# Optimization experiments

Measured on AMD Instinct MI355X. Metric: run time of the kernel, lower is better.

The kernel has to match this reference:

```python
import jax, jax.numpy as jnp
import numpy as np

B, S, D = 4, 2048, 512
H, HD, RL = 8, 64, 64   # nheads, head_dim = D//H, rl_dim
TEMPER = 1.0
BETA = 1.0
SLOPE = 0.01  # LeakyReLU negative slope
LN_EPS = 1e-5


def setup_inputs() -> dict:
    key = jax.random.key(0)
    ks = jax.random.split(key, 12)
    scale = 0.02
    return {
        "h":   jax.random.normal(ks[0], (B, S, D), dtype=jnp.float32),
        "rh":  jax.random.normal(ks[1], (B, S, RL), dtype=jnp.float32),
        "Wl":  jax.random.normal(ks[2], (D, D), dtype=jnp.float32) * scale,   # linear_l (in,out)
        "Wr":  jax.random.normal(ks[3], (D, D), dtype=jnp.float32) * scale,   # linear_r
        "al":  jax.random.normal(ks[4], (HD,), dtype=jnp.float32) * scale,    # att_l: Linear(head_dim,1)
        "ar":  jax.random.normal(ks[5], (HD,), dtype=jnp.float32) * scale,    # att_r
        "Wrs": jax.random.normal(ks[6], (RL, RL * H), dtype=jnp.float32) * scale,  # r_source
        "Wrt": jax.random.normal(ks[7], (RL, RL * H), dtype=jnp.float32) * scale,  # r_target
        "Wf":  jax.random.normal(ks[8], (D, D), dtype=jnp.float32) * scale,   # linear_final
        "ln_g": jnp.ones((D,), dtype=jnp.float32),
        "ln_b": jnp.zeros((D,), dtype=jnp.float32),
    }


def _layer_norm(x, g, b):
    mu = jnp.mean(x, axis=-1, keepdims=True)
    var = jnp.mean(jnp.square(x - mu), axis=-1, keepdims=True)
    return (x - mu) * jax.lax.rsqrt(var + LN_EPS) * g + b


def reference(h, rh, Wl, Wr, al, ar, Wrs, Wrt, Wf, ln_g, ln_b):
    leaky = lambda x: jnp.where(x >= 0, x, SLOPE * x)
    # projections -> [B, H, S, HD]
    fl = (h @ Wl).reshape(B, S, H, HD).transpose(0, 2, 1, 3)
    fr = (h @ Wr).reshape(B, S, H, HD).transpose(0, 2, 1, 3)
    # additive attention logits: [B,H,S,1] + [B,H,1,S]
    sl = jnp.einsum('bhsd,d->bhs', leaky(fl), al)
    sr = jnp.einsum('bhsd,d->bhs', leaky(fr), ar)
    score = sl[:, :, :, None] + sr[:, :, None, :]
    # relation-embedding bilinear bias: r_k @ r_q -> [B,H,S,S]
    r_k = (rh @ Wrs).reshape(B, S, H, RL).transpose(0, 2, 1, 3)   # [B,H,S,RL]
    r_q = (rh @ Wrt).reshape(B, S, H, RL).transpose(0, 2, 3, 1)   # [B,H,RL,S]
    score = score + BETA * jnp.einsum('bhsr,bhrt->bhst', r_k, r_q)
    score = jax.nn.softmax(score / TEMPER, axis=-1)
    # context and output projection (dropout = 0 -> identity)
    context = jnp.einsum('bhst,bhtd->bhsd', score, fr)
    h_sa = context.transpose(0, 2, 1, 3).reshape(B, S, H * HD)
    fh = h_sa @ Wf
    return _layer_norm(h + fh, ln_g, ln_b)
```

## Files before the change

### kernel.cpp

```cpp
#include <hip/hip_runtime.h>
#include <math.h>

#define B_ 4
#define S_ 2048
#define D_ 512
#define H_ 8
#define HD_ 64
#define RL_ 64
#define LN_EPS 1e-5f
#define SLOPE 0.01f
#define LOG2E 1.4426950408889634f

typedef __attribute__((ext_vector_type(8))) __bf16 bf16x8;
typedef __attribute__((ext_vector_type(4))) float f32x4;

__device__ __forceinline__ float leaky(float x) { return x >= 0.f ? x : SLOPE * x; }

__device__ __forceinline__ ushort f2bf(float f) {
    union { float f; unsigned u; } v; v.f = f;
    unsigned r = v.u + 0x7fffu + ((v.u >> 16) & 1u);
    return (ushort)(r >> 16);
}
__device__ __forceinline__ unsigned fbits(float f) {
    union { float f; unsigned u; } v; v.f = f; return v.u;
}

__device__ __forceinline__ void g2lds16(const void* g, void* l) {
    __builtin_amdgcn_global_load_lds(
        (const __attribute__((address_space(1))) void*)(uintptr_t)g,
        (__attribute__((address_space(3))) void*)(uintptr_t)l, 16, 0, 0);
}

__global__ __launch_bounds__(256) void prep(
    const float* __restrict__ h, const float* __restrict__ rh,
    const float* __restrict__ Wr, const float* __restrict__ Wf,
    const float* __restrict__ Wrs, const float* __restrict__ Wrt,
    ushort* __restrict__ hb, ushort* __restrict__ rhb,
    ushort* __restrict__ WrT, ushort* __restrict__ WfT,
    ushort* __restrict__ WrsT, ushort* __restrict__ WrtT)
{
    const int bx = blockIdx.x, tid = threadIdx.x;
    if (bx < 4608) {
        const float* in = (bx < 4096) ? h : rh;
        ushort* o = (bx < 4096) ? hb : rhb;
        const int i = (bx < 4096 ? bx : bx - 4096) * 256 + tid;
        const float4 v = ((const float4*)in)[i];
        ushort4 u; u.x = f2bf(v.x); u.y = f2bf(v.y); u.z = f2bf(v.z); u.w = f2bf(v.w);
        ((ushort4*)o)[i] = u;
        return;
    }
    __shared__ float TS[64][65];
    int t = bx - 4608;
    const float* in; ushort* out; int K, tk, tn;
    if (t < 64)       { in = Wr;  out = WrT;  K = 512; tk = t & 7; tn = t >> 3; }
    else if (t < 128) { in = Wf;  out = WfT;  K = 512; t -= 64; tk = t & 7; tn = t >> 3; }
    else if (t < 136) { in = Wrs; out = WrsT; K = 64;  tk = 0; tn = t - 128; }
    else              { in = Wrt; out = WrtT; K = 64;  tk = 0; tn = t - 136; }
    const int k0 = tk * 64, n0 = tn * 64;
    const int r = tid >> 4, c4 = (tid & 15) * 4;
    #pragma unroll
    for (int p = 0; p < 4; ++p) {
        const int row = r + 16 * p;
        const float4 v = *(const float4*)(in + (size_t)(k0 + row) * 512 + n0 + c4);
        TS[row][c4] = v.x; TS[row][c4 + 1] = v.y;
        TS[row][c4 + 2] = v.z; TS[row][c4 + 3] = v.w;
    }
    __syncthreads();
    #pragma unroll
    for (int p = 0; p < 4; ++p) {
        const int nn = r + 16 * p;
        ushort4 o;
        o.x = f2bf(TS[c4 + 0][nn]); o.y = f2bf(TS[c4 + 1][nn]);
        o.z = f2bf(TS[c4 + 2][nn]); o.w = f2bf(TS[c4 + 3][nn]);
        *(ushort4*)(out + (size_t)(n0 + nn) * K + k0 + c4) = o;
    }
}

__global__ __launch_bounds__(256) void proj(
    const ushort* __restrict__ hb, const ushort* __restrict__ rhb,
    const ushort* __restrict__ WrT, const ushort* __restrict__ WrsT,
    const ushort* __restrict__ WrtT,
    ushort* __restrict__ frT, ushort* __restrict__ rkw, ushort* __restrict__ rqw,
    float* __restrict__ sred, const float* __restrict__ ar)
{
    __shared__ ushort As[2][64 * 32];
    __shared__ ushort Bs[2][128 * 32];

    const int tid = threadIdx.x;
    const int lane = tid & 63, w = tid >> 6;
    const int ln = lane & 15, quad = lane >> 4;
    const int wm = w >> 1, wn = w & 1;
    const int m0 = blockIdx.x * 64, n0 = blockIdx.y * 128;
    const int z = blockIdx.z;

    const ushort* A; const ushort* wt; ushort* co; float scl; int K;
    if (z == 0)      { A = hb;  wt = WrT;  co = frT; scl = LOG2E; K = 512; }
    else if (z == 1) { A = rhb; wt = WrsT; co = rkw; scl = LOG2E; K = 64; }
    else             { A = rhb; wt = WrtT; co = rqw; scl = 1.0f;  K = 64; }

    const int srA = tid >> 2;
    const int lchA = ((lane & 3) - (srA >> 1)) & 3;
    const ushort* AgB = A + (size_t)(m0 + srA) * K + lchA * 8;
    const int srB = w * 32 + (lane >> 2);
    const int lchB = ((lane & 3) - (srB >> 1)) & 3;
    const ushort* BgB0 = wt + (size_t)(n0 + srB) * K + lchB * 8;
    const ushort* BgB1 = BgB0 + (size_t)16 * K;
    const int aoff = tid * 8;
    const int boff = srB * 32 + (lane & 3) * 8;
    const int pc = (quad + (ln >> 1)) & 3;

    g2lds16(AgB, &As[0][aoff]);
    g2lds16(BgB0, &Bs[0][boff]);
    g2lds16(BgB1, &Bs[0][boff + 512]);

    f32x4 acc[2][4] = {};
    int buf = 0;
    for (int k0 = 0; k0 < K; k0 += 32) {
        __syncthreads();
        if (k0 + 32 < K) {
            g2lds16(AgB + k0 + 32, &As[buf ^ 1][aoff]);
            g2lds16(BgB0 + k0 + 32, &Bs[buf ^ 1][boff]);
            g2lds16(BgB1 + k0 + 32, &Bs[buf ^ 1][boff + 512]);
        }
        bf16x8 af[2], bfr[4];
        #pragma unroll
        for (int mi = 0; mi < 2; ++mi)
            af[mi] = *(const bf16x8*)&As[buf][(wm * 32 + mi * 16 + ln) * 32 + pc * 8];
        #pragma unroll
        for (int ni = 0; ni < 4; ++ni)
            bfr[ni] = *(const bf16x8*)&Bs[buf][(wn * 64 + ni * 16 + ln) * 32 + pc * 8];
        #pragma unroll
        for (int mi = 0; mi < 2; ++mi)
            #pragma unroll
            for (int ni = 0; ni < 4; ++ni)
                acc[mi][ni] = __builtin_amdgcn_mfma_f32_16x16x32_bf16(
                    af[mi], bfr[ni], acc[mi][ni], 0, 0, 0);
        buf ^= 1;
    }

    const int head = blockIdx.y * 2 + wn;
    const int b = m0 >> 11;
    const size_t bh = (size_t)b * H_ + head;
    if (z == 0) {
        #pragma unroll
        for (int mi = 0; mi < 2; ++mi) {
            const int s = (m0 & (S_ - 1)) + wm * 32 + mi * 16 + quad * 4;
            #pragma unroll
            for (int ni = 0; ni < 4; ++ni) {
                const int d = ni * 16 + ln;
                ushort4 o;
                o.x = f2bf(acc[mi][ni][0]); o.y = f2bf(acc[mi][ni][1]);
                o.z = f2bf(acc[mi][ni][2]); o.w = f2bf(acc[mi][ni][3]);
                *(ushort4*)(co + (bh * 64 + d) * S_ + s) = o;
            }
        }
        float a4[4];
        #pragma unroll
        for (int ni = 0; ni < 4; ++ni) a4[ni] = ar[ni * 16 + ln];
        #pragma unroll
        for (int mi = 0; mi < 2; ++mi) {
            const int s = (m0 & (S_ - 1)) + wm * 32 + mi * 16 + quad * 4;
            #pragma unroll
            for (int r = 0; r < 4; ++r) {
                float v = 0.f;
                #pragma unroll
                for (int ni = 0; ni < 4; ++ni)
                    v += leaky(acc[mi][ni][r]) * a4[ni];
                #pragma unroll
                for (int off = 8; off; off >>= 1) v += __shfl_xor(v, off, 16);
                if (ln == 0) sred[bh * S_ + s + r] = v * scl;
            }
        }
    } else {
        #pragma unroll
        for (int mi = 0; mi < 2; ++mi) {
            const int s = (m0 & (S_ - 1)) + wm * 32 + mi * 16 + quad * 4;
            #pragma unroll
            for (int ni = 0; ni < 4; ++ni) {
                const int d = ni * 16 + ln;
                #pragma unroll
                for (int r = 0; r < 4; ++r)
                    co[(bh * S_ + s + r) * 64 + d] = f2bf(acc[mi][ni][r] * scl);
            }
        }
    }
}

#define WAITV(N) asm volatile("s_waitcnt vmcnt(" #N ")" ::: "memory")
#define BARR()   __builtin_amdgcn_s_barrier()

__global__ __launch_bounds__(128, 2) void attn_mfma(
    const ushort* __restrict__ frT, const ushort* __restrict__ rk,
    const ushort* __restrict__ rq, const float* __restrict__ sr,
    ushort* __restrict__ hsa)
{
    __shared__ ushort RQ[2][64][64];
    __shared__ ushort FT[2][64][64];
    __shared__ ushort PS[4][16][64];

    const int tid = threadIdx.x;
    const int w = tid >> 6;
    const int lane = tid & 63;
    const int ln = lane & 15;
    const int quad = lane >> 4;

    const int flat = blockIdx.x + 32 * (blockIdx.y + 8 * blockIdx.z);
    const int wid = (flat & 7) * 128 + (flat >> 3);
    const int q0 = (wid & 31) * 64;
    const int h = (wid >> 5) & 7;
    const int b = wid >> 8;
    const size_t bh = (size_t)b * H_ + h;

    bf16x8 a[2][2];
    #pragma unroll
    for (int qs = 0; qs < 2; ++qs) {
        const ushort* p = rk + ((bh * S_ + q0 + 32 * w + 16 * qs + ln) << 6);
        a[qs][0] = *(const bf16x8*)(p + quad * 8);
        a[qs][1] = *(const bf16x8*)(p + 32 + quad * 8);
    }

    const ushort* rq_g = rq + (bh * S_ << 6);
    const ushort* ft_g = frT + (size_t)bh * 64 * S_;
    const float* srp = sr + bh * S_;

    const int rl = lane >> 3;
    const int pg = lane & 7;
    const int base_row = w * 32 + rl;
    const int sgF = (pg - rl) & 7;

    #define STAGE(BUF, t0)                                                    \
        {                                                                     \
            _Pragma("unroll")                                                 \
            for (int m = 0; m < 4; ++m) {                                     \
                const int rr = base_row + 8 * m;                              \
                const int sgR = (pg - ((rr >> 2) & 7)) & 7;                   \
                g2lds16(rq_g + ((size_t)((t0) + rr) << 6) + sgR * 8,          \
                        &RQ[BUF][rr][pg * 8]);                                \
                g2lds16(ft_g + (size_t)rr * S_ + (t0) + sgF * 8,              \
                        &FT[BUF][rr][pg * 8]);                                \
            }                                                                 \
        }

    const ushort* rqrA = &RQ[0][0][0] + 4 * ln * 64 + ((quad + ln) & 7) * 8;
    const ushort* rqrB = &RQ[0][0][0] + 4 * ln * 64 + ((quad + 4 + ln) & 7) * 8;
    const ushort* ftrA = &FT[0][0][0] + ln * 64 + ((quad + ln) & 7) * 8;
    const ushort* ftrB = &FT[0][0][0] + ln * 64 + ((quad + 4 + ln) & 7) * 8;
    ushort* sb[2];
    sb[0] = &PS[w * 2][0][0]; sb[1] = &PS[w * 2 + 1][0][0];
    int wr_off[4];
    #pragma unroll
    for (int r = 0; r < 4; ++r) {
        const int prow = quad * 4 + r;
        wr_off[r] = prow * 64 + (((ln >> 1) + prow) & 7) * 8 + (ln & 1) * 4;
    }
    const int rd0 = ln * 64 + ((quad + ln) & 7) * 8;
    const int rd1 = ln * 64 + ((quad + 4 + ln) & 7) * 8;

    float lsum[2][4] = {};
    f32x4 ctx[2][4] = {};

    #define COMPUTE(BI, SV)                                                        \
        {                                                                          \
            f32x4 sc[2][4];                                                        \
            _Pragma("unroll")                                                      \
            for (int jb = 0; jb < 4; ++jb) {                                       \
                const bf16x8 b0 = *(const bf16x8*)(rqrA + (BI) * 4096 + jb * 64);  \
                const bf16x8 b1 = *(const bf16x8*)(rqrB + (BI) * 4096 + jb * 64);  \
                _Pragma("unroll")                                                  \
                for (int qs = 0; qs < 2; ++qs) {                                   \
                    f32x4 tt = {0.f, 0.f, 0.f, 0.f};                               \
                    tt = __builtin_amdgcn_mfma_f32_16x16x32_bf16(a[qs][0], b0, tt, 0, 0, 0); \
                    tt = __builtin_amdgcn_mfma_f32_16x16x32_bf16(a[qs][1], b1, tt, 0, 0, 0); \
                    sc[qs][jb] = tt;                                               \
                }                                                                  \
            }                                                                      \
            _Pragma("unroll")                                                      \
            for (int qs = 0; qs < 2; ++qs)                                         \
                _Pragma("unroll")                                                  \
                for (int r = 0; r < 4; ++r) {                                      \
                    const float p0 = __builtin_amdgcn_exp2f(sc[qs][0][r] + SV.x);  \
                    const float p1 = __builtin_amdgcn_exp2f(sc[qs][1][r] + SV.y);  \
                    const float p2 = __builtin_amdgcn_exp2f(sc[qs][2][r] + SV.z);  \
                    const float p3 = __builtin_amdgcn_exp2f(sc[qs][3][r] + SV.w);  \
                    lsum[qs][r] += (p0 + p1) + (p2 + p3);                          \
                    const unsigned lo = (fbits(p0) >> 16) | (fbits(p1) & 0xffff0000u); \
                    const unsigned hi = (fbits(p2) >> 16) | (fbits(p3) & 0xffff0000u); \
                    *(uint2*)(sb[qs] + wr_off[r]) = make_uint2(lo, hi);            \
                }                                                                  \
            const bf16x8 pa00 = *(const bf16x8*)(sb[0] + rd0);                     \
            const bf16x8 pa01 = *(const bf16x8*)(sb[0] + rd1);                     \
            const bf16x8 pa10 = *(const bf16x8*)(sb[1] + rd0);                     \
            const bf16x8 pa11 = *(const bf16x8*)(sb[1] + rd1);                     \
            _Pragma("unroll")                                                      \
            for (int jb = 0; jb < 4; ++jb) {                                       \
                const bf16x8 fb0 = *(const bf16x8*)(ftrA + (BI) * 4096 + jb * 1024); \
                const bf16x8 fb1 = *(const bf16x8*)(ftrB + (BI) * 4096 + jb * 1024); \
                ctx[0][jb] = __builtin_amdgcn_mfma_f32_16x16x32_bf16(pa00, fb0, ctx[0][jb], 0, 0, 0); \
                ctx[0][jb] = __builtin_amdgcn_mfma_f32_16x16x32_bf16(pa01, fb1, ctx[0][jb], 0, 0, 0); \
                ctx[1][jb] = __builtin_amdgcn_mfma_f32_16x16x32_bf16(pa10, fb0, ctx[1][jb], 0, 0, 0); \
                ctx[1][jb] = __builtin_amdgcn_mfma_f32_16x16x32_bf16(pa11, fb1, ctx[1][jb], 0, 0, 0); \
            }                                                                      \
        }

    float4 sv0, sv1;
    STAGE(0, 0)  sv0 = *(const float4*)(srp + 0 + 4 * ln);

    for (int it = 0; it < 15; ++it) {
        const int t0 = it * 128;
        WAITV(0); BARR();
        STAGE(1, t0 + 64)   sv1 = *(const float4*)(srp + t0 + 64 + 4 * ln);
        COMPUTE(0, sv0)
        WAITV(0); BARR();
        STAGE(0, t0 + 128)  sv0 = *(const float4*)(srp + t0 + 128 + 4 * ln);
        COMPUTE(1, sv1)
    }
    WAITV(0); BARR();
    STAGE(1, 1984)  sv1 = *(const float4*)(srp + 1984 + 4 * ln);
    COMPUTE(0, sv0)
    WAITV(0); BARR();
    COMPUTE(1, sv1)

    #pragma unroll
    for (int qs = 0; qs < 2; ++qs)
        #pragma unroll
        for (int r = 0; r < 4; ++r) {
            float l = lsum[qs][r];
            #pragma unroll
            for (int off = 8; off; off >>= 1) l += __shfl_xor(l, off, 16);
            const float inv = 1.f / l;
            const int q = q0 + 32 * w + 16 * qs + quad * 4 + r;
            ushort* orow = hsa + (size_t)(b * S_ + q) * D_ + h * 64;
            #pragma unroll
            for (int jb = 0; jb < 4; ++jb)
                orow[16 * jb + ln] = f2bf(ctx[qs][jb][r] * inv);
        }
}

__global__ __launch_bounds__(256) void gemm_out(
    const ushort* __restrict__ A, const ushort* __restrict__ WT,
    float* __restrict__ C)
{
    __shared__ ushort As[2][64 * 32];
    __shared__ ushort Bs[2][128 * 32];

    const int tid = threadIdx.x;
    const int lane = tid & 63, w = tid >> 6;
    const int ln = lane & 15, quad = lane >> 4;
    const int wm = w >> 1, wn = w & 1;
    const int m0 = blockIdx.x * 64, n0 = blockIdx.y * 128;
    const int K = 512;

    const int srA = tid >> 2;
    const int lchA = ((lane & 3) - (srA >> 1)) & 3;
    const ushort* AgB = A + (size_t)(m0 + srA) * K + lchA * 8;
    const int srB = w * 32 + (lane >> 2);
    const int lchB = ((lane & 3) - (srB >> 1)) & 3;
    const ushort* BgB0 = WT + (size_t)(n0 + srB) * K + lchB * 8;
    const ushort* BgB1 = BgB0 + (size_t)16 * K;
    const int aoff = tid * 8;
    const int boff = srB * 32 + (lane & 3) * 8;
    const int pc = (quad + (ln >> 1)) & 3;

    g2lds16(AgB, &As[0][aoff]);
    g2lds16(BgB0, &Bs[0][boff]);
    g2lds16(BgB1, &Bs[0][boff + 512]);

    f32x4 acc[2][4] = {};
    int buf = 0;
    for (int k0 = 0; k0 < K; k0 += 32) {
        __syncthreads();
        if (k0 + 32 < K) {
            g2lds16(AgB + k0 + 32, &As[buf ^ 1][aoff]);
            g2lds16(BgB0 + k0 + 32, &Bs[buf ^ 1][boff]);
            g2lds16(BgB1 + k0 + 32, &Bs[buf ^ 1][boff + 512]);
        }
        bf16x8 af[2], bfr[4];
        #pragma unroll
        for (int mi = 0; mi < 2; ++mi)
            af[mi] = *(const bf16x8*)&As[buf][(wm * 32 + mi * 16 + ln) * 32 + pc * 8];
        #pragma unroll
        for (int ni = 0; ni < 4; ++ni)
            bfr[ni] = *(const bf16x8*)&Bs[buf][(wn * 64 + ni * 16 + ln) * 32 + pc * 8];
        #pragma unroll
        for (int mi = 0; mi < 2; ++mi)
            #pragma unroll
            for (int ni = 0; ni < 4; ++ni)
                acc[mi][ni] = __builtin_amdgcn_mfma_f32_16x16x32_bf16(
                    af[mi], bfr[ni], acc[mi][ni], 0, 0, 0);
        buf ^= 1;
    }

    #pragma unroll
    for (int mi = 0; mi < 2; ++mi) {
        const int row = m0 + wm * 32 + mi * 16 + quad * 4;
        #pragma unroll
        for (int ni = 0; ni < 4; ++ni) {
            const int col = n0 + wn * 64 + ni * 16 + ln;
            #pragma unroll
            for (int r = 0; r < 4; ++r)
                C[(size_t)(row + r) * 512 + col] = acc[mi][ni][r];
        }
    }
}

__global__ __launch_bounds__(256) void ln_kernel(
    const float* __restrict__ h, const float* __restrict__ fh,
    const float* __restrict__ g, const float* __restrict__ bb,
    float* __restrict__ out)
{
    const int row = blockIdx.x, tid = threadIdx.x;
    const float* hp = h + (size_t)row * 512;
    const float* fp = fh + (size_t)row * 512;
    const float x0 = hp[tid] + fp[tid];
    const float x1 = hp[tid + 256] + fp[tid + 256];
    __shared__ float red[4];

    float s = x0 + x1;
    #pragma unroll
    for (int off = 32; off; off >>= 1) s += __shfl_xor(s, off, 64);
    if ((tid & 63) == 0) red[tid >> 6] = s;
    __syncthreads();
    const float mu = (red[0] + red[1] + red[2] + red[3]) * (1.f / 512.f);

    const float d0 = x0 - mu, d1 = x1 - mu;
    float v = d0 * d0 + d1 * d1;
    #pragma unroll
    for (int off = 32; off; off >>= 1) v += __shfl_xor(v, off, 64);
    __syncthreads();
    if ((tid & 63) == 0) red[tid >> 6] = v;
    __syncthreads();
    const float var = (red[0] + red[1] + red[2] + red[3]) * (1.f / 512.f);
    const float inv = rsqrtf(var + LN_EPS);

    out[(size_t)row * 512 + tid] = d0 * inv * g[tid] + bb[tid];
    out[(size_t)row * 512 + tid + 256] = d1 * inv * g[tid + 256] + bb[tid + 256];
}

extern "C" void kernel_launch(void* const* d_in, const int* in_sizes, int n_in,
                              void* d_out, int out_size, void* d_ws, size_t ws_size,
                              hipStream_t stream)
{
    const float* h   = (const float*)d_in[0];
    const float* rh  = (const float*)d_in[1];
    const float* Wr  = (const float*)d_in[3];
    const float* ar  = (const float*)d_in[5];
    const float* Wrs = (const float*)d_in[6];
    const float* Wrt = (const float*)d_in[7];
    const float* Wf  = (const float*)d_in[8];
    const float* lng = (const float*)d_in[9];
    const float* lnb = (const float*)d_in[10];
    float* out = (float*)d_out;
    char* wsb  = (char*)d_ws;

    const size_t MB = (size_t)1 << 20;
    ushort* hb   = (ushort*)(wsb);
    ushort* rhb  = (ushort*)(wsb + 8 * MB);
    ushort* WrT  = (ushort*)(wsb + 9 * MB);
    ushort* WfT  = (ushort*)(wsb + 9 * MB + 512 * 1024);
    ushort* WrsT = (ushort*)(wsb + 10 * MB);
    ushort* WrtT = (ushort*)(wsb + 10 * MB + 64 * 1024);
    ushort* frT  = (ushort*)(wsb + 11 * MB);
    ushort* rkw  = (ushort*)(wsb + 19 * MB);
    ushort* rqw  = (ushort*)(wsb + 27 * MB);
    float*  sr   = (float*) (wsb + 35 * MB);
    ushort* hsab = (ushort*)(wsb + 36 * MB);
    float*  fh   = (float*) (wsb + 44 * MB);

    dim3 blk(256);
    prep<<<dim3(4752), blk, 0, stream>>>(h, rh, Wr, Wf, Wrs, Wrt,
                                         hb, rhb, WrT, WfT, WrsT, WrtT);
    proj<<<dim3(128, 4, 3), blk, 0, stream>>>(hb, rhb, WrT, WrsT, WrtT,
                                              frT, rkw, rqw, sr, ar);
    attn_mfma<<<dim3(S_ / 64, H_, B_), dim3(128), 0, stream>>>(frT, rkw, rqw, sr, hsab);
    gemm_out<<<dim3(128, 4), blk, 0, stream>>>(hsab, WfT, fh);
    ln_kernel<<<dim3(B_ * S_), blk, 0, stream>>>(h, fh, lng, lnb, out);
}
```

Measured before the change: 176.7 us.

## Rewrite attention core with 32x32x16 MFMA and register-resident probabilities

The attention kernel moves from 16x16x32 to 32x32x16 bf16 MFMA tiles. Each wave now handles 64 queries, and each block handles 128 queries, so the grid is halved. Score tiles are computed transposed so the exponentiated probabilities can be packed to bf16 and fed straight into the P@V MFMA through a permlane32 swap, instead of a round trip through LDS. The projection kernel permutes its frT store order to match the new operand layout. This adds register pressure and drops the launch-bounds occupancy hint from 2 to 1, with fewer blocks available to hide latency.

Result: slower. 197.2 us (+11.6%).

```diff
diff --git a/kernel.cpp b/kernel.cpp
--- a/kernel.cpp
+++ b/kernel.cpp
@@ -13,6 +13,7 @@
 
 typedef __attribute__((ext_vector_type(8))) __bf16 bf16x8;
 typedef __attribute__((ext_vector_type(4))) float f32x4;
+typedef __attribute__((ext_vector_type(16))) float f32x16;
 
 __device__ __forceinline__ float leaky(float x) { return x >= 0.f ? x : SLOPE * x; }
 
@@ -21,14 +22,18 @@
     unsigned r = v.u + 0x7fffu + ((v.u >> 16) & 1u);
     return (ushort)(r >> 16);
 }
-__device__ __forceinline__ unsigned fbits(float f) {
-    union { float f; unsigned u; } v; v.f = f; return v.u;
+__device__ __forceinline__ unsigned pk2bf(float a, float b) {
+    return (unsigned)f2bf(a) | ((unsigned)f2bf(b) << 16);
 }
 
 __device__ __forceinline__ void g2lds16(const void* g, void* l) {
     __builtin_amdgcn_global_load_lds(
         (const __attribute__((address_space(1))) void*)(uintptr_t)g,
         (__attribute__((address_space(3))) void*)(uintptr_t)l, 16, 0, 0);
+}
+
+__device__ __forceinline__ void plane32swap(unsigned &x, unsigned &y) {
+    asm volatile("v_permlane32_swap_b32 %0, %1" : "+v"(x), "+v"(y));
 }
 
 __global__ __launch_bounds__(256) void prep(
@@ -145,13 +150,14 @@
         #pragma unroll
         for (int mi = 0; mi < 2; ++mi) {
             const int s = (m0 & (S_ - 1)) + wm * 32 + mi * 16 + quad * 4;
+            const int sp = (s & ~15) | ((((0x1320u >> (quad * 4)) & 0xFu)) << 2);
             #pragma unroll
             for (int ni = 0; ni < 4; ++ni) {
                 const int d = ni * 16 + ln;
                 ushort4 o;
                 o.x = f2bf(acc[mi][ni][0]); o.y = f2bf(acc[mi][ni][1]);
                 o.z = f2bf(acc[mi][ni][2]); o.w = f2bf(acc[mi][ni][3]);
-                *(ushort4*)(co + (bh * 64 + d) * S_ + s) = o;
+                *(ushort4*)(co + (bh * 64 + d) * S_ + sp) = o;
             }
         }
         float a4[4];
@@ -189,151 +195,147 @@
 #define WAITV(N) asm volatile("s_waitcnt vmcnt(" #N ")" ::: "memory")
 #define BARR()   __builtin_amdgcn_s_barrier()
 
-__global__ __launch_bounds__(128, 2) void attn_mfma(
+__global__ __launch_bounds__(128, 1) void attn_mfma(
     const ushort* __restrict__ frT, const ushort* __restrict__ rk,
     const ushort* __restrict__ rq, const float* __restrict__ sr,
     ushort* __restrict__ hsa)
 {
     __shared__ ushort RQ[2][64][64];
     __shared__ ushort FT[2][64][64];
-    __shared__ ushort PS[4][16][64];
 
     const int tid = threadIdx.x;
     const int w = tid >> 6;
     const int lane = tid & 63;
-    const int ln = lane & 15;
-    const int quad = lane >> 4;
-
-    const int flat = blockIdx.x + 32 * (blockIdx.y + 8 * blockIdx.z);
-    const int wid = (flat & 7) * 128 + (flat >> 3);
-    const int q0 = (wid & 31) * 64;
-    const int h = (wid >> 5) & 7;
-    const int b = wid >> 8;
+    const int lq = lane & 31;
+    const int hi = lane >> 5;
+
+    const int flat = blockIdx.x + 16 * (blockIdx.y + 8 * blockIdx.z);
+    const int wid = (flat & 7) * 64 + (flat >> 3);
+    const int q0 = (wid & 15) * 128;
+    const int h = (wid >> 4) & 7;
+    const int b = wid >> 7;
     const size_t bh = (size_t)b * H_ + h;
-
-    bf16x8 a[2][2];
-    #pragma unroll
-    for (int qs = 0; qs < 2; ++qs) {
-        const ushort* p = rk + ((bh * S_ + q0 + 32 * w + 16 * qs + ln) << 6);
-        a[qs][0] = *(const bf16x8*)(p + quad * 8);
-        a[qs][1] = *(const bf16x8*)(p + 32 + quad * 8);
+    const int qb = q0 + 64 * w;
+
+    bf16x8 bq[2][4];
+    #pragma unroll
+    for (int qt = 0; qt < 2; ++qt) {
+        const ushort* p = rk + ((bh * S_ + qb + 32 * qt + lq) << 6) + hi * 8;
+        #pragma unroll
+        for (int ks = 0; ks < 4; ++ks)
+            bq[qt][ks] = *(const bf16x8*)(p + ks * 16);
     }
 
     const ushort* rq_g = rq + (bh * S_ << 6);
     const ushort* ft_g = frT + (size_t)bh * 64 * S_;
     const float* srp = sr + bh * S_;
 
-    const int rl = lane >> 3;
-    const int pg = lane & 7;
-    const int base_row = w * 32 + rl;
-    const int sgF = (pg - rl) & 7;
+    const int srow = tid >> 3;
+    const int pg = tid & 7;
+    const int oS = (pg - (srow & 7)) & 7;
 
     #define STAGE(BUF, t0)                                                    \
-        {                                                                     \
-            _Pragma("unroll")                                                 \
-            for (int m = 0; m < 4; ++m) {                                     \
-                const int rr = base_row + 8 * m;                              \
-                const int sgR = (pg - ((rr >> 2) & 7)) & 7;                   \
-                g2lds16(rq_g + ((size_t)((t0) + rr) << 6) + sgR * 8,          \
-                        &RQ[BUF][rr][pg * 8]);                                \
-                g2lds16(ft_g + (size_t)rr * S_ + (t0) + sgF * 8,              \
-                        &FT[BUF][rr][pg * 8]);                                \
-            }                                                                 \
-        }
-
-    const ushort* rqrA = &RQ[0][0][0] + 4 * ln * 64 + ((quad + ln) & 7) * 8;
-    const ushort* rqrB = &RQ[0][0][0] + 4 * ln * 64 + ((quad + 4 + ln) & 7) * 8;
-    const ushort* ftrA = &FT[0][0][0] + ln * 64 + ((quad + ln) & 7) * 8;
-    const ushort* ftrB = &FT[0][0][0] + ln * 64 + ((quad + 4 + ln) & 7) * 8;
-    ushort* sb[2];
-    sb[0] = &PS[w * 2][0][0]; sb[1] = &PS[w * 2 + 1][0][0];
-    int wr_off[4];
-    #pragma unroll
-    for (int r = 0; r < 4; ++r) {
-        const int prow = quad * 4 + r;
-        wr_off[r] = prow * 64 + (((ln >> 1) + prow) & 7) * 8 + (ln & 1) * 4;
-    }
-    const int rd0 = ln * 64 + ((quad + ln) & 7) * 8;
-    const int rd1 = ln * 64 + ((quad + 4 + ln) & 7) * 8;
-
-    float lsum[2][4] = {};
-    f32x4 ctx[2][4] = {};
-
-    #define COMPUTE(BI, SV)                                                        \
-        {                                                                          \
-            f32x4 sc[2][4];                                                        \
-            _Pragma("unroll")                                                      \
-            for (int jb = 0; jb < 4; ++jb) {                                       \
-                const bf16x8 b0 = *(const bf16x8*)(rqrA + (BI) * 4096 + jb * 64);  \
-                const bf16x8 b1 = *(const bf16x8*)(rqrB + (BI) * 4096 + jb * 64);  \
-                _Pragma("unroll")                                                  \
-                for (int qs = 0; qs < 2; ++qs) {                                   \
-                    f32x4 tt = {0.f, 0.f, 0.f, 0.f};                               \
-                    tt = __builtin_amdgcn_mfma_f32_16x16x32_bf16(a[qs][0], b0, tt, 0, 0, 0); \
-                    tt = __builtin_amdgcn_mfma_f32_16x16x32_bf16(a[qs][1], b1, tt, 0, 0, 0); \
-                    sc[qs][jb] = tt;                                               \
-                }                                                                  \
-            }                                                                      \
-            _Pragma("unroll")                                                      \
-            for (int qs = 0; qs < 2; ++qs)                                         \
-                _Pragma("unroll")                                                  \
-                for (int r = 0; r < 4; ++r) {                                      \
-                    const float p0 = __builtin_amdgcn_exp2f(sc[qs][0][r] + SV.x);  \
-                    const float p1 = __builtin_amdgcn_exp2f(sc[qs][1][r] + SV.y);  \
-                    const float p2 = __builtin_amdgcn_exp2f(sc[qs][2][r] + SV.z);  \
-                    const float p3 = __builtin_amdgcn_exp2f(sc[qs][3][r] + SV.w);  \
-                    lsum[qs][r] += (p0 + p1) + (p2 + p3);                          \
-                    const unsigned lo = (fbits(p0) >> 16) | (fbits(p1) & 0xffff0000u); \
-                    const unsigned hi = (fbits(p2) >> 16) | (fbits(p3) & 0xffff0000u); \
-                    *(uint2*)(sb[qs] + wr_off[r]) = make_uint2(lo, hi);            \
-                }                                                                  \
-            const bf16x8 pa00 = *(const bf16x8*)(sb[0] + rd0);                     \
-            const bf16x8 pa01 = *(const bf16x8*)(sb[0] + rd1);                     \
-            const bf16x8 pa10 = *(const bf16x8*)(sb[1] + rd0);                     \
-            const bf16x8 pa11 = *(const bf16x8*)(sb[1] + rd1);                     \
-            _Pragma("unroll")                                                      \
-            for (int jb = 0; jb < 4; ++jb) {                                       \
-                const bf16x8 fb0 = *(const bf16x8*)(ftrA + (BI) * 4096 + jb * 1024); \
-                const bf16x8 fb1 = *(const bf16x8*)(ftrB + (BI) * 4096 + jb * 1024); \
-                ctx[0][jb] = __builtin_amdgcn_mfma_f32_16x16x32_bf16(pa00, fb0, ctx[0][jb], 0, 0, 0); \
-                ctx[0][jb] = __builtin_amdgcn_mfma_f32_16x16x32_bf16(pa01, fb1, ctx[0][jb], 0, 0, 0); \
-                ctx[1][jb] = __builtin_amdgcn_mfma_f32_16x16x32_bf16(pa10, fb0, ctx[1][jb], 0, 0, 0); \
-                ctx[1][jb] = __builtin_amdgcn_mfma_f32_16x16x32_bf16(pa11, fb1, ctx[1][jb], 0, 0, 0); \
-            }                                                                      \
-        }
-
-    float4 sv0, sv1;
-    STAGE(0, 0)  sv0 = *(const float4*)(srp + 0 + 4 * ln);
-
+        { _Pragma("unroll")                                                   \
+          for (int j = 0; j < 4; ++j) {                                       \
+            const int rr = 16 * j + srow;                                     \
+            g2lds16(rq_g + ((size_t)((t0) + rr) << 6) + oS * 8,               \
+                    &RQ[BUF][rr][pg * 8]);                                    \
+            g2lds16(ft_g + (size_t)rr * S_ + (t0) + oS * 8,                   \
+                    &FT[BUF][rr][pg * 8]);                                    \
+          } }
+
+    f32x16 ctx[2][2] = {};
+    float lsum[2] = {0.f, 0.f};
+
+    #define COMPUTE(BI, TC)                                                    \
+    {                                                                          \
+        uint4 paw[2][4];                                                       \
+        _Pragma("unroll")                                                      \
+        for (int tt = 0; tt < 2; ++tt) {                                       \
+            bf16x8 af[4];                                                      \
+            _Pragma("unroll")                                                  \
+            for (int ks = 0; ks < 4; ++ks)                                     \
+                af[ks] = *(const bf16x8*)(&RQ[BI][0][0] + (tt * 32 + lq) * 64  \
+                           + ((2 * ks + hi + (lq & 7)) & 7) * 8);              \
+            f32x16 s0 = {}; f32x16 s1 = {};                                    \
+            _Pragma("unroll")                                                  \
+            for (int ks = 0; ks < 4; ++ks) {                                   \
+                s0 = __builtin_amdgcn_mfma_f32_32x32x16_bf16(af[ks], bq[0][ks], s0, 0, 0, 0); \
+                s1 = __builtin_amdgcn_mfma_f32_32x32x16_bf16(af[ks], bq[1][ks], s1, 0, 0, 0); \
+            }                                                                  \
+            float sva[16];                                                     \
+            _Pragma("unroll")                                                  \
+            for (int jj = 0; jj < 4; ++jj) {                                   \
+                const float4 v = *(const float4*)(srp + (TC) + tt * 32 + jj * 8 + hi * 4); \
+                sva[jj * 4 + 0] = v.x; sva[jj * 4 + 1] = v.y;                  \
+                sva[jj * 4 + 2] = v.z; sva[jj * 4 + 3] = v.w;                  \
+            }                                                                  \
+            _Pragma("unroll")                                                  \
+            for (int qt = 0; qt < 2; ++qt) {                                   \
+                float p[16];                                                   \
+                _Pragma("unroll")                                              \
+                for (int r = 0; r < 16; ++r)                                   \
+                    p[r] = __builtin_amdgcn_exp2f((qt ? s1[r] : s0[r]) + sva[r]); \
+                float ls = 0.f;                                                \
+                _Pragma("unroll")                                              \
+                for (int r = 0; r < 16; ++r) ls += p[r];                       \
+                lsum[qt] += ls;                                                \
+                _Pragma("unroll")                                              \
+                for (int c = 0; c < 2; ++c) {                                  \
+                    const int e = 8 * c;                                       \
+                    unsigned c01 = pk2bf(p[e + 0], p[e + 1]);                  \
+                    unsigned c23 = pk2bf(p[e + 2], p[e + 3]);                  \
+                    unsigned c45 = pk2bf(p[e + 4], p[e + 5]);                  \
+                    unsigned c67 = pk2bf(p[e + 6], p[e + 7]);                  \
+                    plane32swap(c45, c67);   \
+                    paw[qt][tt * 2 + c] = make_uint4(c01, c23, c67, c45);      \
+                }                                                              \
+            }                                                                  \
+        }                                                                      \
+        _Pragma("unroll")                                                      \
+        for (int ts = 0; ts < 4; ++ts) {                                       \
+            _Pragma("unroll")                                                  \
+            for (int dt = 0; dt < 2; ++dt) {                                   \
+                const bf16x8 fv = *(const bf16x8*)(&FT[BI][0][0]               \
+                    + (dt * 32 + lq) * 64 + ((2 * ts + hi + (lq & 7)) & 7) * 8); \
+                ctx[0][dt] = __builtin_amdgcn_mfma_f32_32x32x16_bf16(          \
+                    __builtin_bit_cast(bf16x8, paw[0][ts]), fv, ctx[0][dt], 0, 0, 0); \
+                ctx[1][dt] = __builtin_amdgcn_mfma_f32_32x32x16_bf16(          \
+                    __builtin_bit_cast(bf16x8, paw[1][ts]), fv, ctx[1][dt], 0, 0, 0); \
+            }                                                                  \
+        }                                                                      \
+    }
+
+    STAGE(0, 0)
     for (int it = 0; it < 15; ++it) {
         const int t0 = it * 128;
         WAITV(0); BARR();
-        STAGE(1, t0 + 64)   sv1 = *(const float4*)(srp + t0 + 64 + 4 * ln);
-        COMPUTE(0, sv0)
+        STAGE(1, t0 + 64)
+        COMPUTE(0, t0)
         WAITV(0); BARR();
-        STAGE(0, t0 + 128)  sv0 = *(const float4*)(srp + t0 + 128 + 4 * ln);
-        COMPUTE(1, sv1)
+        STAGE(0, t0 + 128)
+        COMPUTE(1, t0 + 64)
     }
     WAITV(0); BARR();
-    STAGE(1, 1984)  sv1 = *(const float4*)(srp + 1984 + 4 * ln);
-    COMPUTE(0, sv0)
+    STAGE(1, 1984)
+    COMPUTE(0, 1920)
     WAITV(0); BARR();
-    COMPUTE(1, sv1)
-
-    #pragma unroll
-    for (int qs = 0; qs < 2; ++qs)
-        #pragma unroll
-        for (int r = 0; r < 4; ++r) {
-            float l = lsum[qs][r];
-            #pragma unroll
-            for (int off = 8; off; off >>= 1) l += __shfl_xor(l, off, 16);
-            const float inv = 1.f / l;
-            const int q = q0 + 32 * w + 16 * qs + quad * 4 + r;
-            ushort* orow = hsa + (size_t)(b * S_ + q) * D_ + h * 64;
-            #pragma unroll
-            for (int jb = 0; jb < 4; ++jb)
-                orow[16 * jb + ln] = f2bf(ctx[qs][jb][r] * inv);
-        }
+    COMPUTE(1, 1984)
+
+    #pragma unroll
+    for (int qt = 0; qt < 2; ++qt) {
+        const float l = lsum[qt] + __shfl_xor(lsum[qt], 32, 64);
+        const float inv = 1.f / l;
+        #pragma unroll
+        for (int r = 0; r < 16; ++r) {
+            const int rho = (r & 3) + 8 * (r >> 2) + 4 * hi;
+            const float fi = __shfl(inv, rho, 64);
+            const int q = qb + 32 * qt + rho;
+            ushort* orow = hsa + (size_t)(b * S_ + q) * D_ + h * 64 + lq;
+            orow[0]  = f2bf(ctx[qt][0][r] * fi);
+            orow[32] = f2bf(ctx[qt][1][r] * fi);
+        }
+    }
 }
 
 __global__ __launch_bounds__(256) void gemm_out(
@@ -471,7 +473,7 @@
                                          hb, rhb, WrT, WfT, WrsT, WrtT);
     proj<<<dim3(128, 4, 3), blk, 0, stream>>>(hb, rhb, WrT, WrsT, WrtT,
                                               frT, rkw, rqw, sr, ar);
-    attn_mfma<<<dim3(S_ / 64, H_, B_), dim3(128), 0, stream>>>(frT, rkw, rqw, sr, hsab);
+    attn_mfma<<<dim3(S_ / 128, H_, B_), dim3(128), 0, stream>>>(frT, rkw, rqw, sr, hsab);
     gemm_out<<<dim3(128, 4), blk, 0, stream>>>(hsab, WfT, fh);
     ln_kernel<<<dim3(B_ * S_), blk, 0, stream>>>(h, fh, lng, lnb, out);
 }
```
